# Kernel tuning notes

Measured on AMD Instinct MI355X. Metric: run time of the kernel, lower is better.

Reference implementation:

```python
import jax, jax.numpy as jnp
import numpy as np

T = 1000
C = 3
H = 64
W = 64
N_ITER = 3  # fixed-point iterations standing in for the DEQ solver


def _make_coeffs():
    # DDIM coefficient precompute, mirroring get_ddim_injection with sddim=False
    betas = np.linspace(1e-4, 0.02, T, dtype=np.float64)
    # compute_alpha prepends beta_0 = 0, so alphabar has length T+1 with alphabar[0]=1
    alphabar = np.cumprod(np.concatenate([[1.0], 1.0 - betas]))
    t = np.arange(T - 1, -1, -1)            # cur_seq[::-1] = [T-1, ..., 0]
    at = alphabar[t + 1]                    # alphabar indexed at t+1
    at_next = alphabar[t]                   # next_t = t-1  ->  alphabar[next_t+1]
    alpha_ratio = np.sqrt(at_next / at[0])
    et_coeff2 = np.sqrt(1.0 - at_next) - np.sqrt((1.0 - at) * at_next / at)
    et_coeff = et_coeff2 / np.sqrt(at_next)
    et_prevsum_coeff = np.sqrt(at_next)
    rs = lambda a: jnp.asarray(a.reshape(T, 1, 1, 1), dtype=jnp.float32)
    return rs(alpha_ratio), rs(et_coeff), rs(et_prevsum_coeff), jnp.asarray(t, dtype=jnp.int32)


def setup_inputs() -> dict:
    key = jax.random.key(0)
    k1, k2, k3 = jax.random.split(key, 3)
    alpha_ratio, et_coeff, et_prevsum_coeff, t = _make_coeffs()
    x = jax.random.normal(k1, (T + 1, C, H, W), dtype=jnp.float32)
    conv_w = jax.random.normal(k2, (C, C, 3, 3), dtype=jnp.float32) * 0.1
    temb = jax.random.normal(k3, (T, C), dtype=jnp.float32) * 0.1
    return {"x": x, "t": t, "alpha_ratio": alpha_ratio, "et_coeff": et_coeff,
            "et_prevsum_coeff": et_prevsum_coeff, "conv_w": conv_w, "temb": temb}


def _model(xt_in, t, conv_w, temb):
    # epsilon model stand-in: 3x3 conv + per-timestep channel bias
    y = jax.lax.conv_general_dilated(
        xt_in, conv_w, window_strides=(1, 1), padding="SAME",
        dimension_numbers=("NCHW", "OIHW", "NCHW"))
    return y + temb[t][:, :, None, None]


def reference(x, t, alpha_ratio, et_coeff, et_prevsum_coeff, conv_w, temb):
    xT = x[0:1]                                   # [1,C,H,W]
    all_xT = alpha_ratio * xT                     # broadcast == repeat_interleave then scale -> [T,C,H,W]

    def func(xt):
        xt_in = xt[:T]                            # gather via next_idx = [0..T-1]
        et = _model(xt_in, t, conv_w, temb)
        et_updated = et_coeff * et
        et_prevsum = jnp.cumsum(et_updated, axis=0)
        xt_next = all_xT + et_prevsum_coeff * et_prevsum
        # scatter: xt_all[xT_idx]=xT, xt_all[prev_idx]=xt_next  (xT_idx=[0], prev_idx=[1..T])
        return jnp.concatenate([xT, xt_next], axis=0)

    xt = x
    for _ in range(N_ITER):
        xt = func(xt)
    return xt
```

## Files before the change

kernel.cpp:

```cpp
#include <hip/hip_runtime.h>

#define TT 1000
#define CC 3
#define HH 64
#define WW 64
#define HW 4096
#define CHW 12288
#define CHW4 3072
#define NCHUNK 50
#define CLEN 20
#define NCONVB 2000

__device__ __forceinline__ float bf2f(unsigned short u) {
    return __uint_as_float(((unsigned)u) << 16);
}
__device__ __forceinline__ unsigned short f2bf(float f) {
    unsigned u = __float_as_uint(f);
    return (unsigned short)((u + 0x7FFFu + ((u >> 16) & 1u)) >> 16);
}

template <bool IN_BF16, bool COPY_TAIL>
__global__ __launch_bounds__(256) void conv_kernel(const void* __restrict__ xin_v,
                                                   const float* __restrict__ cw,
                                                   const float* __restrict__ temb,
                                                   const int* __restrict__ tarr,
                                                   const float* __restrict__ ec,
                                                   unsigned short* __restrict__ A,
                                                   float* __restrict__ out0,
                                                   unsigned short* __restrict__ X0) {
    if (COPY_TAIL && blockIdx.x >= NCONVB) {
        int i = (blockIdx.x - NCONVB) * 256 + threadIdx.x;
        if (i < CHW4) {
            float4 v = ((const float4*)xin_v)[i];
            ((float4*)out0)[i] = v;
            ushort4 u;
            u.x = f2bf(v.x); u.y = f2bf(v.y); u.z = f2bf(v.z); u.w = f2bf(v.w);
            *(ushort4*)(X0 + (size_t)i * 4) = u;
        }
        return;
    }

    int idx = blockIdx.x * 256 + threadIdx.x;
    int wi = idx & 15;
    int hp = (idx >> 4) & 31;
    int t  = idx >> 9;
    int h0 = hp * 2;
    int w0 = wi * 4;

    const float* xtf = (const float*)xin_v + (size_t)t * CHW;
    const unsigned short* xtb = (const unsigned short*)xin_v + (size_t)t * CHW;

    float acc[2][CC][4];
    #pragma unroll
    for (int o = 0; o < 2; ++o)
        #pragma unroll
        for (int co = 0; co < CC; ++co)
            #pragma unroll
            for (int k = 0; k < 4; ++k) acc[o][co][k] = 0.f;

    #pragma unroll
    for (int ch = 0; ch < CC; ++ch) {
        #pragma unroll
        for (int j = 0; j < 4; ++j) {
            int h = h0 - 1 + j;
            bool hv = (unsigned)h < (unsigned)HH;
            float4 M;
            if (IN_BF16) {
                ushort4 u = make_ushort4(0, 0, 0, 0);
                if (hv) u = *(const ushort4*)(xtb + ch * HW + h * WW + w0);
                M = make_float4(bf2f(u.x), bf2f(u.y), bf2f(u.z), bf2f(u.w));
            } else {
                M = hv ? *(const float4*)(xtf + ch * HW + h * WW + w0)
                       : make_float4(0.f, 0.f, 0.f, 0.f);
            }
            float left  = __shfl_up(M.w, 1);    if (wi == 0)  left  = 0.f;
            float right = __shfl_down(M.x, 1);  if (wi == 15) right = 0.f;
            float win[6] = {left, M.x, M.y, M.z, M.w, right};
            #pragma unroll
            for (int o = 0; o < 2; ++o) {
                const int kh = j - o;
                if (kh >= 0 && kh <= 2) {
                    #pragma unroll
                    for (int co = 0; co < CC; ++co) {
                        float wa = cw[((co * CC + ch) * 3 + kh) * 3 + 0];
                        float wb = cw[((co * CC + ch) * 3 + kh) * 3 + 1];
                        float wc = cw[((co * CC + ch) * 3 + kh) * 3 + 2];
                        #pragma unroll
                        for (int k = 0; k < 4; ++k)
                            acc[o][co][k] += win[k] * wa + win[k + 1] * wb + win[k + 2] * wc;
                    }
                }
            }
        }
    }

    float e = ec[t];
    int tr = tarr[t];
    #pragma unroll
    for (int o = 0; o < 2; ++o)
        #pragma unroll
        for (int co = 0; co < CC; ++co) {
            float b = temb[tr * CC + co];
            ushort4 v;
            v.x = f2bf(e * (acc[o][co][0] + b));
            v.y = f2bf(e * (acc[o][co][1] + b));
            v.z = f2bf(e * (acc[o][co][2] + b));
            v.w = f2bf(e * (acc[o][co][3] + b));
            *(ushort4*)(A + (size_t)t * CHW + co * HW + (h0 + o) * WW + w0) = v;
        }
}

__global__ __launch_bounds__(256) void chunk_sum_kernel(const unsigned short* __restrict__ A,
                                                        float4* __restrict__ S) {
    int ch = blockIdx.x / 12;
    int pos4 = (blockIdx.x % 12) * 256 + threadIdx.x;
    const unsigned short* p = A + (size_t)ch * CLEN * CHW + pos4 * 4;
    float4 acc = make_float4(0.f, 0.f, 0.f, 0.f);
    #pragma unroll
    for (int i = 0; i < CLEN; ++i) {
        ushort4 u = *(const ushort4*)(p + (size_t)i * CHW);
        acc.x += bf2f(u.x); acc.y += bf2f(u.y); acc.z += bf2f(u.z); acc.w += bf2f(u.w);
    }
    S[(size_t)ch * CHW4 + pos4] = acc;
}

template <bool OUT_BF16>
__global__ __launch_bounds__(256) void final_kernel(const unsigned short* __restrict__ A,
                                                    const float4* __restrict__ S,
                                                    const float4* __restrict__ xT,
                                                    const float* __restrict__ ar,
                                                    const float* __restrict__ epc,
                                                    void* __restrict__ out_v) {
    int ch = blockIdx.x / 12;
    int pos4 = (blockIdx.x % 12) * 256 + threadIdx.x;

    float4 a0 = make_float4(0.f, 0.f, 0.f, 0.f);
    float4 a1 = make_float4(0.f, 0.f, 0.f, 0.f);
    float4 a2 = make_float4(0.f, 0.f, 0.f, 0.f);
    float4 a3 = make_float4(0.f, 0.f, 0.f, 0.f);
    int j = 0;
    for (; j + 4 <= ch; j += 4) {
        float4 v0 = S[(size_t)(j + 0) * CHW4 + pos4];
        float4 v1 = S[(size_t)(j + 1) * CHW4 + pos4];
        float4 v2 = S[(size_t)(j + 2) * CHW4 + pos4];
        float4 v3 = S[(size_t)(j + 3) * CHW4 + pos4];
        a0.x += v0.x; a0.y += v0.y; a0.z += v0.z; a0.w += v0.w;
        a1.x += v1.x; a1.y += v1.y; a1.z += v1.z; a1.w += v1.w;
        a2.x += v2.x; a2.y += v2.y; a2.z += v2.z; a2.w += v2.w;
        a3.x += v3.x; a3.y += v3.y; a3.z += v3.z; a3.w += v3.w;
    }
    for (; j < ch; ++j) {
        float4 v = S[(size_t)j * CHW4 + pos4];
        a0.x += v.x; a0.y += v.y; a0.z += v.z; a0.w += v.w;
    }
    float4 acc = make_float4((a0.x + a1.x) + (a2.x + a3.x),
                             (a0.y + a1.y) + (a2.y + a3.y),
                             (a0.z + a1.z) + (a2.z + a3.z),
                             (a0.w + a1.w) + (a2.w + a3.w));

    float4 xv = xT[pos4];
    const unsigned short* p = A + (size_t)ch * CLEN * CHW + pos4 * 4;
    float4* qf = (float4*)out_v + (size_t)(ch * CLEN + 1) * CHW4 + pos4;
    unsigned short* qb = (unsigned short*)out_v + ((size_t)(ch * CLEN + 1) * CHW4 + pos4) * 4;
    #pragma unroll
    for (int i = 0; i < CLEN; ++i) {
        int t = ch * CLEN + i;
        ushort4 u = *(const ushort4*)(p + (size_t)i * CHW);
        acc.x += bf2f(u.x); acc.y += bf2f(u.y); acc.z += bf2f(u.z); acc.w += bf2f(u.w);
        float a = ar[t], e = epc[t];
        float4 r = make_float4(a * xv.x + e * acc.x, a * xv.y + e * acc.y,
                               a * xv.z + e * acc.z, a * xv.w + e * acc.w);
        if (OUT_BF16) {
            ushort4 ub;
            ub.x = f2bf(r.x); ub.y = f2bf(r.y); ub.z = f2bf(r.z); ub.w = f2bf(r.w);
            *(ushort4*)(qb + (size_t)i * CHW) = ub;
        } else {
            qf[(size_t)i * CHW4] = r;
        }
    }
}

extern "C" void kernel_launch(void* const* d_in, const int* in_sizes, int n_in,
                              void* d_out, int out_size, void* d_ws, size_t ws_size,
                              hipStream_t stream) {
    const float* x    = (const float*)d_in[0];
    const int*   tarr = (const int*)  d_in[1];
    const float* ar   = (const float*)d_in[2];
    const float* ec   = (const float*)d_in[3];
    const float* epc  = (const float*)d_in[4];
    const float* cw   = (const float*)d_in[5];
    const float* temb = (const float*)d_in[6];
    float* out = (float*)d_out;

    unsigned short* A = (unsigned short*)d_ws;
    float* S = (float*)(A + (size_t)TT * CHW);
    unsigned short* X = (unsigned short*)(S + (size_t)NCHUNK * CHW);

    conv_kernel<false, true><<<NCONVB + 12, 256, 0, stream>>>(x, cw, temb, tarr, ec, A, out, X);
    chunk_sum_kernel<<<NCHUNK * 12, 256, 0, stream>>>(A, (float4*)S);
    final_kernel<true><<<NCHUNK * 12, 256, 0, stream>>>(A, (const float4*)S,
                                                        (const float4*)x, ar, epc, X);

    conv_kernel<true, false><<<NCONVB, 256, 0, stream>>>(X, cw, temb, tarr, ec, A, out, X);
    chunk_sum_kernel<<<NCHUNK * 12, 256, 0, stream>>>(A, (float4*)S);
    final_kernel<true><<<NCHUNK * 12, 256, 0, stream>>>(A, (const float4*)S,
                                                        (const float4*)x, ar, epc, X);

    conv_kernel<true, false><<<NCONVB, 256, 0, stream>>>(X, cw, temb, tarr, ec, A, out, X);
    chunk_sum_kernel<<<NCHUNK * 12, 256, 0, stream>>>(A, (float4*)S);
    final_kernel<false><<<NCHUNK * 12, 256, 0, stream>>>(A, (const float4*)S,
                                                         (const float4*)x, ar, epc, out);
}
```

Before: 203.0 us.

## Compute four output rows per thread with packed f32x2 conv math and nontemporal stores

Each conv thread now produces four output rows instead of two, with one block per timestep. Six input rows are loaded for four outputs instead of four for two, which cuts redundant input loads and shuffles. Accumulation uses two-wide float vectors so the compiler can emit packed FMA instructions. The final fp32 output writes in the scan kernel become nontemporal stores to avoid polluting the cache. The costs are higher register pressure, now capped by a launch-bounds occupancy hint of 4, and half as many conv blocks.

```diff
diff --git a/kernel.cpp b/kernel.cpp
--- a/kernel.cpp
+++ b/kernel.cpp
@@ -9,7 +9,10 @@
 #define CHW4 3072
 #define NCHUNK 50
 #define CLEN 20
-#define NCONVB 2000
+#define NCONVB 1000
+
+typedef float f32x2 __attribute__((ext_vector_type(2)));
+typedef float f32x4 __attribute__((ext_vector_type(4)));
 
 __device__ __forceinline__ float bf2f(unsigned short u) {
     return __uint_as_float(((unsigned)u) << 16);
@@ -20,14 +23,14 @@
 }
 
 template <bool IN_BF16, bool COPY_TAIL>
-__global__ __launch_bounds__(256) void conv_kernel(const void* __restrict__ xin_v,
-                                                   const float* __restrict__ cw,
-                                                   const float* __restrict__ temb,
-                                                   const int* __restrict__ tarr,
-                                                   const float* __restrict__ ec,
-                                                   unsigned short* __restrict__ A,
-                                                   float* __restrict__ out0,
-                                                   unsigned short* __restrict__ X0) {
+__global__ __launch_bounds__(256, 4) void conv_kernel(const void* __restrict__ xin_v,
+                                                      const float* __restrict__ cw,
+                                                      const float* __restrict__ temb,
+                                                      const int* __restrict__ tarr,
+                                                      const float* __restrict__ ec,
+                                                      unsigned short* __restrict__ A,
+                                                      float* __restrict__ out0,
+                                                      unsigned short* __restrict__ X0) {
     if (COPY_TAIL && blockIdx.x >= NCONVB) {
         int i = (blockIdx.x - NCONVB) * 256 + threadIdx.x;
         if (i < CHW4) {
@@ -40,28 +43,29 @@
         return;
     }
 
-    int idx = blockIdx.x * 256 + threadIdx.x;
-    int wi = idx & 15;
-    int hp = (idx >> 4) & 31;
-    int t  = idx >> 9;
-    int h0 = hp * 2;
+    int tid = threadIdx.x;
+    int wi = tid & 15;
+    int hr = tid >> 4;
     int w0 = wi * 4;
+    int h0 = hr * 4;
+    int t  = blockIdx.x;
 
     const float* xtf = (const float*)xin_v + (size_t)t * CHW;
     const unsigned short* xtb = (const unsigned short*)xin_v + (size_t)t * CHW;
 
-    float acc[2][CC][4];
-    #pragma unroll
-    for (int o = 0; o < 2; ++o)
+    f32x2 acc[4][CC][2];
+    #pragma unroll
+    for (int o = 0; o < 4; ++o)
         #pragma unroll
-        for (int co = 0; co < CC; ++co)
-            #pragma unroll
-            for (int k = 0; k < 4; ++k) acc[o][co][k] = 0.f;
+        for (int co = 0; co < CC; ++co) {
+            acc[o][co][0] = (f32x2){0.f, 0.f};
+            acc[o][co][1] = (f32x2){0.f, 0.f};
+        }
 
     #pragma unroll
     for (int ch = 0; ch < CC; ++ch) {
         #pragma unroll
-        for (int j = 0; j < 4; ++j) {
+        for (int j = 0; j < 6; ++j) {
             int h = h0 - 1 + j;
             bool hv = (unsigned)h < (unsigned)HH;
             float4 M;
@@ -75,9 +79,13 @@
             }
             float left  = __shfl_up(M.w, 1);    if (wi == 0)  left  = 0.f;
             float right = __shfl_down(M.x, 1);  if (wi == 15) right = 0.f;
-            float win[6] = {left, M.x, M.y, M.z, M.w, right};
+            f32x2 P0 = {left, M.x};
+            f32x2 P1 = {M.x,  M.y};
+            f32x2 P2 = {M.y,  M.z};
+            f32x2 P3 = {M.z,  M.w};
+            f32x2 P4 = {M.w,  right};
             #pragma unroll
-            for (int o = 0; o < 2; ++o) {
+            for (int o = 0; o < 4; ++o) {
                 const int kh = j - o;
                 if (kh >= 0 && kh <= 2) {
                     #pragma unroll
@@ -85,9 +93,8 @@
                         float wa = cw[((co * CC + ch) * 3 + kh) * 3 + 0];
                         float wb = cw[((co * CC + ch) * 3 + kh) * 3 + 1];
                         float wc = cw[((co * CC + ch) * 3 + kh) * 3 + 2];
-                        #pragma unroll
-                        for (int k = 0; k < 4; ++k)
-                            acc[o][co][k] += win[k] * wa + win[k + 1] * wb + win[k + 2] * wc;
+                        acc[o][co][0] += P0 * wa + P1 * wb + P2 * wc;
+                        acc[o][co][1] += P2 * wa + P3 * wb + P4 * wc;
                     }
                 }
             }
@@ -97,15 +104,15 @@
     float e = ec[t];
     int tr = tarr[t];
     #pragma unroll
-    for (int o = 0; o < 2; ++o)
+    for (int o = 0; o < 4; ++o)
         #pragma unroll
         for (int co = 0; co < CC; ++co) {
             float b = temb[tr * CC + co];
             ushort4 v;
-            v.x = f2bf(e * (acc[o][co][0] + b));
-            v.y = f2bf(e * (acc[o][co][1] + b));
-            v.z = f2bf(e * (acc[o][co][2] + b));
-            v.w = f2bf(e * (acc[o][co][3] + b));
+            v.x = f2bf(e * (acc[o][co][0].x + b));
+            v.y = f2bf(e * (acc[o][co][0].y + b));
+            v.z = f2bf(e * (acc[o][co][1].x + b));
+            v.w = f2bf(e * (acc[o][co][1].y + b));
             *(ushort4*)(A + (size_t)t * CHW + co * HW + (h0 + o) * WW + w0) = v;
         }
 }
@@ -160,7 +167,7 @@
 
     float4 xv = xT[pos4];
     const unsigned short* p = A + (size_t)ch * CLEN * CHW + pos4 * 4;
-    float4* qf = (float4*)out_v + (size_t)(ch * CLEN + 1) * CHW4 + pos4;
+    float* qf = (float*)out_v + ((size_t)(ch * CLEN + 1) * CHW4 + pos4) * 4;
     unsigned short* qb = (unsigned short*)out_v + ((size_t)(ch * CLEN + 1) * CHW4 + pos4) * 4;
     #pragma unroll
     for (int i = 0; i < CLEN; ++i) {
@@ -175,7 +182,8 @@
             ub.x = f2bf(r.x); ub.y = f2bf(r.y); ub.z = f2bf(r.z); ub.w = f2bf(r.w);
             *(ushort4*)(qb + (size_t)i * CHW) = ub;
         } else {
-            qf[(size_t)i * CHW4] = r;
+            f32x4 rv = {r.x, r.y, r.z, r.w};
+            __builtin_nontemporal_store(rv, (f32x4*)(qf + (size_t)i * CHW));
         }
     }
 }
```

Result: slower. 242.6 us (+19.5%).
